# Optimization experiments

Measured on AMD Instinct MI355X. Metric: run time of the kernel, lower is better.

The kernel has to match this reference:

```python
import jax, jax.numpy as jnp
import numpy as np

DIM = 1024
N_HEAD = 16
N_KV_HEAD = 4
HEAD_DIM = DIM // N_HEAD  # 64
INTER = 2688
B, N = 2, 2048
EPS = 1e-6


def setup_inputs() -> dict:
    key = jax.random.key(0)
    ks = jax.random.split(key, 10)
    std = 0.02
    x = jax.random.normal(ks[0], (B, N, DIM), dtype=jnp.float32)
    # rotary embedding: theta = pos * 10000^(-2i/d), cos/sin of shape [N, HEAD_DIM//2]
    inv_freq = 1.0 / (10000.0 ** (np.arange(0, HEAD_DIM, 2, dtype=np.float32) / HEAD_DIM))
    t = np.arange(N, dtype=np.float32)
    ang = np.outer(t, inv_freq)  # [N, HEAD_DIM//2]
    rope_cos = jnp.asarray(np.cos(ang))
    rope_sin = jnp.asarray(np.sin(ang))
    mask = jnp.tril(jnp.ones((N, N), dtype=bool))  # True = attend
    return {
        "x": x,
        "w_attn_norm": jnp.ones((DIM,), jnp.float32),
        "w_ffn_norm": jnp.ones((DIM,), jnp.float32),
        "Wq": jax.random.normal(ks[1], (DIM, N_HEAD * HEAD_DIM), jnp.float32) * std,
        "Wkv": jax.random.normal(ks[2], (DIM, 2 * N_KV_HEAD * HEAD_DIM), jnp.float32) * std,
        "Wo": jax.random.normal(ks[3], (N_HEAD * HEAD_DIM, DIM), jnp.float32) * std,
        "W1": jax.random.normal(ks[4], (DIM, INTER), jnp.float32) * std,
        "W2": jax.random.normal(ks[5], (INTER, DIM), jnp.float32) * std,
        "W3": jax.random.normal(ks[6], (DIM, INTER), jnp.float32) * std,
        "rope_cos": rope_cos,
        "rope_sin": rope_sin,
        "mask": mask,
    }


def _rms_norm(x, w):
    # nn.functional.rms_norm: x / sqrt(mean(x^2) + eps) * w
    return x * jax.lax.rsqrt(jnp.mean(x * x, axis=-1, keepdims=True) + EPS) * w


def _apply_rope(x, cos, sin):
    # x: [b, n, h, d]; consecutive pairs (x[2k], x[2k+1]) form complex numbers
    xr = x[..., 0::2]
    xi = x[..., 1::2]
    c = cos[None, :, None, :]
    s = sin[None, :, None, :]
    yr = xr * c - xi * s
    yi = xr * s + xi * c
    return jnp.stack([yr, yi], axis=-1).reshape(x.shape)


def _block(x, w_attn_norm, w_ffn_norm, Wq, Wkv, Wo, W1, W2, W3, rope_cos, rope_sin, mask):
    b, n, _ = x.shape
    # --- attention (GQA, use_cache=False prefill) ---
    h = _rms_norm(x, w_attn_norm)
    q = (h @ Wq).reshape(b, n, N_HEAD, HEAD_DIM)
    kv = h @ Wkv
    k, v = jnp.split(kv, 2, axis=-1)
    k = k.reshape(b, n, N_KV_HEAD, HEAD_DIM)
    v = v.reshape(b, n, N_KV_HEAD, HEAD_DIM)
    q = _apply_rope(q, rope_cos, rope_sin)
    k = _apply_rope(k, rope_cos, rope_sin)
    # einops repeat 'b n h d -> b n (r h) d' == tile along head axis
    r = N_HEAD // N_KV_HEAD
    k = jnp.tile(k, (1, 1, r, 1))
    v = jnp.tile(v, (1, 1, r, 1))
    scale = HEAD_DIM ** -0.5
    scores = jnp.einsum('bnhd,bmhd->bhnm', q, k) * scale
    scores = jnp.where(mask[None, None, :, :], scores, jnp.finfo(scores.dtype).min)
    attn = jax.nn.softmax(scores, axis=-1)
    o = jnp.einsum('bhnm,bmhd->bnhd', attn, v).reshape(b, n, N_HEAD * HEAD_DIM)
    x = x + o @ Wo
    # --- SwiGLU MLP ---
    h2 = _rms_norm(x, w_ffn_norm)
    ff = (jax.nn.silu(h2 @ W1) * (h2 @ W3)) @ W2
    return x + ff


def reference(x, w_attn_norm, w_ffn_norm, Wq, Wkv, Wo, W1, W2, W3, rope_cos, rope_sin, mask):
    return _block(x, w_attn_norm, w_ffn_norm, Wq, Wkv, Wo, W1, W2, W3, rope_cos, rope_sin, mask)
```

## Files before the change

### kernel.cpp

```cpp
#include <hip/hip_runtime.h>

#define DIM 1024
#define NH 16
#define NKV 4
#define HD 64
#define INTER 2688
#define BB 2
#define NN 2048
#define MM (BB*NN)

typedef __attribute__((ext_vector_type(4))) float f32x4;
typedef __attribute__((ext_vector_type(16))) float f32x16;
typedef __attribute__((ext_vector_type(8))) short short8;

#define CROW(r,h) ((((r)&3)) + 8*((r)>>2) + 4*(h))

__device__ __forceinline__ unsigned short f2bf(float f) {
  union { float f; unsigned u; } v; v.f = f;
  unsigned r = v.u + 0x7fffu + ((v.u >> 16) & 1u);
  return (unsigned short)(r >> 16);
}

__device__ __forceinline__ void glds16(const unsigned short* g, unsigned short* l) {
  __builtin_amdgcn_global_load_lds(
      (const __attribute__((address_space(1))) void*)g,
      (__attribute__((address_space(3))) void*)l, 16, 0, 0);
}

__device__ __forceinline__ void xcd_map(int& bx, int& by) {
  int gx = gridDim.x;
  int nwg = gx * gridDim.y;
  int bid = (int)blockIdx.y * gx + (int)blockIdx.x;
  int cpx = nwg >> 3;
  int lg = (bid & 7) * cpx + (bid >> 3);
  bx = lg % gx;
  by = lg / gx;
}

__global__ void transpose_all(const float* __restrict__ Wq, const float* __restrict__ Wkv,
                              const float* __restrict__ Wo, const float* __restrict__ W1,
                              const float* __restrict__ W3, const float* __restrict__ W2,
                              unsigned short* __restrict__ WqkvT, unsigned short* __restrict__ WoT,
                              unsigned short* __restrict__ W1T, unsigned short* __restrict__ W3T,
                              unsigned short* __restrict__ W2T) {
  int tb = blockIdx.x;
  const float* src; unsigned short* dst; int K, Nc, t0;
  if (tb < 1024)        { src = Wq;  dst = WqkvT;                         K = 1024; Nc = 1024; t0 = tb; }
  else if (tb < 1536)   { src = Wkv; dst = WqkvT + (size_t)1024 * 1024;   K = 1024; Nc = 512;  t0 = tb - 1024; }
  else if (tb < 2560)   { src = Wo;  dst = WoT;                           K = 1024; Nc = 1024; t0 = tb - 1536; }
  else if (tb < 5248)   { src = W1;  dst = W1T;                           K = 1024; Nc = 2688; t0 = tb - 2560; }
  else if (tb < 7936)   { src = W3;  dst = W3T;                           K = 1024; Nc = 2688; t0 = tb - 5248; }
  else                  { src = W2;  dst = W2T;                           K = 2688; Nc = 1024; t0 = tb - 7936; }
  int ntx = Nc >> 5;
  int n0 = (t0 % ntx) * 32, k0 = (t0 / ntx) * 32;
  __shared__ float tile[32][33];
  int tx = threadIdx.x & 31, ty = threadIdx.x >> 5;
#pragma unroll
  for (int i = 0; i < 32; i += 8)
    tile[ty + i][tx] = src[(size_t)(k0 + ty + i) * Nc + n0 + tx];
  __syncthreads();
#pragma unroll
  for (int i = 0; i < 32; i += 8)
    dst[(size_t)(n0 + ty + i) * K + k0 + tx] = f2bf(tile[tx][ty + i]);
}

__global__ void rmsnorm_k(const float* __restrict__ x, const float* __restrict__ w,
                          unsigned short* __restrict__ h) {
  int row = blockIdx.x;
  int t = threadIdx.x;
  const float4* xr = (const float4*)(x + (size_t)row * DIM);
  float4 v = xr[t];
  float ss = v.x * v.x + v.y * v.y + v.z * v.z + v.w * v.w;
#pragma unroll
  for (int o = 1; o < 64; o <<= 1) ss += __shfl_xor(ss, o);
  __shared__ float ps[4];
  if ((t & 63) == 0) ps[t >> 6] = ss;
  __syncthreads();
  float r = rsqrtf((ps[0] + ps[1] + ps[2] + ps[3]) * (1.0f / DIM) + 1e-6f);
  const float4* wr = (const float4*)w;
  float4 wv = wr[t];
  ushort4 o4;
  o4.x = f2bf(v.x * r * wv.x);
  o4.y = f2bf(v.y * r * wv.y);
  o4.z = f2bf(v.z * r * wv.z);
  o4.w = f2bf(v.w * r * wv.w);
  *(ushort4*)(h + (size_t)row * DIM + t * 4) = o4;
}

template <bool RES>
__global__ __launch_bounds__(256, 4) void gemm64(
    const unsigned short* __restrict__ A, const unsigned short* __restrict__ Bt,
    const float* __restrict__ res, float* __restrict__ C, int Nc, int K) {
  __shared__ __align__(16) unsigned short Asm[2][64 * 32];
  __shared__ __align__(16) unsigned short Bsm[2][128 * 32];
  int tid = threadIdx.x;
  int w = tid >> 6, l = tid & 63;
  int bx, by;
  xcd_map(bx, by);
  int bm = by * 64, bn = bx * 128;
  int wc = w * 32;
  int c0 = l & 15, g = l >> 4;

  int sra = w * 16 + (l >> 2);
  int srb = w * 32 + (l >> 2);
  int sca = ((l & 3) ^ ((sra >> 1) & 3)) * 8;
  int scb = ((l & 3) ^ ((srb >> 1) & 3)) * 8;
  const unsigned short* gA  = A + (size_t)(bm + sra) * K + sca;
  const unsigned short* gB0 = Bt + (size_t)(bn + srb) * K + scb;
  const unsigned short* gB1 = Bt + (size_t)(bn + srb + 16) * K + scb;
  int lsa = (w * 16) * 32, lsb0 = (w * 32) * 32, lsb1 = (w * 32 + 16) * 32;

  int aoff[4], boff[2];
#pragma unroll
  for (int m = 0; m < 4; m++) {
    int ra = m * 16 + c0;
    aoff[m] = ra * 32 + (g ^ ((ra >> 1) & 3)) * 8;
  }
#pragma unroll
  for (int n = 0; n < 2; n++) {
    int rb = wc + n * 16 + c0;
    boff[n] = rb * 32 + (g ^ ((rb >> 1) & 3)) * 8;
  }

  f32x4 acc[4][2] = {};
  int T = K / 32;
  glds16(gA, &Asm[0][lsa]);
  glds16(gB0, &Bsm[0][lsb0]);
  glds16(gB1, &Bsm[0][lsb1]);
  __syncthreads();
  int buf = 0;
  for (int s = 0; s < T; ++s) {
    int nb = buf ^ 1;
    if (s + 1 < T) {
      int ko = (s + 1) * 32;
      glds16(gA + ko, &Asm[nb][lsa]);
      glds16(gB0 + ko, &Bsm[nb][lsb0]);
      glds16(gB1 + ko, &Bsm[nb][lsb1]);
    }
    const unsigned short* As = Asm[buf];
    const unsigned short* Bs = Bsm[buf];
    short8 af[4], bf[2];
#pragma unroll
    for (int m = 0; m < 4; m++) af[m] = *(const short8*)&As[aoff[m]];
#pragma unroll
    for (int n = 0; n < 2; n++) bf[n] = *(const short8*)&Bs[boff[n]];
    __builtin_amdgcn_s_setprio(1);
#pragma unroll
    for (int m = 0; m < 4; m++)
#pragma unroll
      for (int n = 0; n < 2; n++)
        acc[m][n] = __builtin_amdgcn_mfma_f32_16x16x32_bf16(af[m], bf[n], acc[m][n], 0, 0, 0);
    __builtin_amdgcn_s_setprio(0);
    __syncthreads();
    buf = nb;
  }
  int gq = l >> 4;
#pragma unroll
  for (int m = 0; m < 4; m++) {
#pragma unroll
    for (int i = 0; i < 4; i++) {
      int row = bm + m * 16 + gq * 4 + i;
#pragma unroll
      for (int n = 0; n < 2; n++) {
        int col = bn + wc + n * 16 + c0;
        float v = acc[m][n][i];
        if (RES) v += res[(size_t)row * Nc + col];
        C[(size_t)row * Nc + col] = v;
      }
    }
  }
}

__global__ __launch_bounds__(256, 4) void gemm_qkv(
    const unsigned short* __restrict__ A, const unsigned short* __restrict__ Bt,
    const float* __restrict__ cosb, const float* __restrict__ sinb,
    unsigned short* __restrict__ qb, unsigned short* __restrict__ kb,
    unsigned short* __restrict__ vtb) {
  const int K = 1024;
  const float QS = 0.125f * 1.44269504f;
  __shared__ __align__(16) unsigned short Asm[2][64 * 32];
  __shared__ __align__(16) unsigned short Bsm[2][128 * 32];
  int tid = threadIdx.x;
  int w = tid >> 6, l = tid & 63;
  int bx, by;
  xcd_map(bx, by);
  int bm = by * 64, bn = bx * 128;
  int wc = w * 32;
  int c0 = l & 15, g = l >> 4;

  int sra = w * 16 + (l >> 2);
  int srb = w * 32 + (l >> 2);
  int sca = ((l & 3) ^ ((sra >> 1) & 3)) * 8;
  int scb = ((l & 3) ^ ((srb >> 1) & 3)) * 8;
  const unsigned short* gA  = A + (size_t)(bm + sra) * K + sca;
  const unsigned short* gB0 = Bt + (size_t)(bn + srb) * K + scb;
  const unsigned short* gB1 = Bt + (size_t)(bn + srb + 16) * K + scb;
  int lsa = (w * 16) * 32, lsb0 = (w * 32) * 32, lsb1 = (w * 32 + 16) * 32;

  int aoff[4], boff[2];
#pragma unroll
  for (int m = 0; m < 4; m++) {
    int ra = m * 16 + c0;
    aoff[m] = ra * 32 + (g ^ ((ra >> 1) & 3)) * 8;
  }
#pragma unroll
  for (int n = 0; n < 2; n++) {
    int rb = wc + n * 16 + c0;
    boff[n] = rb * 32 + (g ^ ((rb >> 1) & 3)) * 8;
  }

  f32x4 acc[4][2] = {};
  int T = K / 32;
  glds16(gA, &Asm[0][lsa]);
  glds16(gB0, &Bsm[0][lsb0]);
  glds16(gB1, &Bsm[0][lsb1]);
  __syncthreads();
  int buf = 0;
  for (int s = 0; s < T; ++s) {
    int nb = buf ^ 1;
    if (s + 1 < T) {
      int ko = (s + 1) * 32;
      glds16(gA + ko, &Asm[nb][lsa]);
      glds16(gB0 + ko, &Bsm[nb][lsb0]);
      glds16(gB1 + ko, &Bsm[nb][lsb1]);
    }
    const unsigned short* As = Asm[buf];
    const unsigned short* Bs = Bsm[buf];
    short8 af[4], bf[2];
#pragma unroll
    for (int m = 0; m < 4; m++) af[m] = *(const short8*)&As[aoff[m]];
#pragma unroll
    for (int n = 0; n < 2; n++) bf[n] = *(const short8*)&Bs[boff[n]];
    __builtin_amdgcn_s_setprio(1);
#pragma unroll
    for (int m = 0; m < 4; m++)
#pragma unroll
      for (int n = 0; n < 2; n++)
        acc[m][n] = __builtin_amdgcn_mfma_f32_16x16x32_bf16(af[m], bf[n], acc[m][n], 0, 0, 0);
    __builtin_amdgcn_s_setprio(0);
    __syncthreads();
    buf = nb;
  }
  int gq = l >> 4;
  int lodd = c0 & 1;
#pragma unroll
  for (int m = 0; m < 4; m++) {
#pragma unroll
    for (int i = 0; i < 4; i++) {
      int row = bm + m * 16 + gq * 4 + i;
      int b = row >> 11, tok = row & (NN - 1);
#pragma unroll
      for (int n = 0; n < 2; n++) {
        int col = bn + wc + n * 16 + c0;
        float val = acc[m][n][i];
        float partner = __shfl_xor(val, 1);
        if (bn < 1024) {
          int head = col >> 6, d = col & 63, j = d >> 1;
          float c = cosb[tok * 32 + j], s = sinb[tok * 32 + j];
          float r = lodd ? (partner * s + val * c) : (val * c - partner * s);
          qb[(((size_t)(b * NH + head)) * NN + tok) * 64 + d] = f2bf(r * QS);
        } else if (bn < 1280) {
          int cc = col - 1024;
          int kvh = cc >> 6, d = cc & 63, j = d >> 1;
          float c = cosb[tok * 32 + j], s = sinb[tok * 32 + j];
          float r = lodd ? (partner * s + val * c) : (val * c - partner * s);
          kb[(((size_t)(b * NKV + kvh)) * NN + tok) * 64 + d] = f2bf(r);
        } else {
          int cc = col - 1280;
          int kvh = cc >> 6, d = cc & 63;
          vtb[(((size_t)(b * NKV + kvh)) * 64 + d) * NN + tok] = f2bf(val);
        }
      }
    }
  }
}

__global__ __launch_bounds__(256, 3) void gemm_ffn13(
    const unsigned short* __restrict__ A, const unsigned short* __restrict__ B1t,
    const unsigned short* __restrict__ B3t, unsigned short* __restrict__ G,
    int Nc, int K) {
  __shared__ __align__(16) unsigned short Asm[2 * 128 * 32];
  __shared__ __align__(16) unsigned short B1sm[2 * 64 * 32];
  __shared__ __align__(16) unsigned short B3sm[2 * 64 * 32];
  int tid = threadIdx.x;
  int w = tid >> 6, l = tid & 63;
  int bm = blockIdx.y * 128, bn = blockIdx.x * 64;
  int wr = (w >> 1) * 64, wc = (w & 1) * 32;
  int c0 = l & 15, g = l >> 4;

  int sr = w * 32 + (l >> 2);
  int sb = w * 16 + (l >> 2);
  int sc  = ((l & 3) ^ ((sr >> 1) & 3)) * 8;
  int scb = ((l & 3) ^ ((sb >> 1) & 3)) * 8;
  const unsigned short* gA0 = A + (size_t)(bm + sr) * K + sc;
  const unsigned short* gA1 = A + (size_t)(bm + sr + 16) * K + sc;
  const unsigned short* gB1 = B1t + (size_t)(bn + sb) * K + scb;
  const unsigned short* gB3 = B3t + (size_t)(bn + sb) * K + scb;
  int ls0 = (w * 32) * 32, ls1 = (w * 32 + 16) * 32, lsb = (w * 16) * 32;

  int aoff[4], boff[2];
#pragma unroll
  for (int m = 0; m < 4; m++) {
    int ra = wr + m * 16 + c0;
    aoff[m] = ra * 32 + (g ^ ((ra >> 1) & 3)) * 8;
  }
#pragma unroll
  for (int n = 0; n < 2; n++) {
    int rb = wc + n * 16 + c0;
    boff[n] = rb * 32 + (g ^ ((rb >> 1) & 3)) * 8;
  }

  f32x4 a1[4][2] = {};
  f32x4 a3[4][2] = {};
  int nsteps = K / 32;
  glds16(gA0, &Asm[ls0]);
  glds16(gA1, &Asm[ls1]);
  glds16(gB1, &B1sm[lsb]);
  glds16(gB3, &B3sm[lsb]);
  __syncthreads();
  int buf = 0;
  for (int s = 0; s < nsteps; ++s) {
    int nb = buf ^ 1;
    if (s + 1 < nsteps) {
      int ko = (s + 1) * 32;
      glds16(gA0 + ko, &Asm[nb * 4096 + ls0]);
      glds16(gA1 + ko, &Asm[nb * 4096 + ls1]);
      glds16(gB1 + ko, &B1sm[nb * 2048 + lsb]);
      glds16(gB3 + ko, &B3sm[nb * 2048 + lsb]);
    }
    const unsigned short* As = &Asm[buf * 4096];
    const unsigned short* B1s = &B1sm[buf * 2048];
    const unsigned short* B3s = &B3sm[buf * 2048];
    short8 af[4], b1f[2], b3f[2];
#pragma unroll
    for (int m = 0; m < 4; m++) af[m] = *(const short8*)&As[aoff[m]];
#pragma unroll
    for (int n = 0; n < 2; n++) {
      b1f[n] = *(const short8*)&B1s[boff[n]];
      b3f[n] = *(const short8*)&B3s[boff[n]];
    }
    __builtin_amdgcn_s_setprio(1);
#pragma unroll
    for (int m = 0; m < 4; m++)
#pragma unroll
      for (int n = 0; n < 2; n++) {
        a1[m][n] = __builtin_amdgcn_mfma_f32_16x16x32_bf16(af[m], b1f[n], a1[m][n], 0, 0, 0);
        a3[m][n] = __builtin_amdgcn_mfma_f32_16x16x32_bf16(af[m], b3f[n], a3[m][n], 0, 0, 0);
      }
    __builtin_amdgcn_s_setprio(0);
    __syncthreads();
    buf = nb;
  }
  int gq = l >> 4;
#pragma unroll
  for (int m = 0; m < 4; m++) {
#pragma unroll
    for (int i = 0; i < 4; i++) {
      int row = bm + wr + m * 16 + gq * 4 + i;
#pragma unroll
      for (int n = 0; n < 2; n++) {
        int col = bn + wc + n * 16 + c0;
        float x1 = a1[m][n][i], x3 = a3[m][n][i];
        float sg = x1 / (1.0f + __expf(-x1));
        G[(size_t)row * Nc + col] = f2bf(sg * x3);
      }
    }
  }
}

__global__ __launch_bounds__(256, 3) void attn_k(
    const unsigned short* __restrict__ qg_, const unsigned short* __restrict__ kg_,
    const unsigned short* __restrict__ vg_, unsigned short* __restrict__ ob) {
  __shared__ __align__(16) unsigned short Ksm[2][64 * 64];
  __shared__ __align__(16) unsigned short Vsm[2][64 * 64];
  int qb = (blockIdx.z == 0) ? (int)blockIdx.x : ((int)gridDim.x - 1 - (int)blockIdx.x);
  int h = blockIdx.y, b = blockIdx.z;
  int kvh = h & 3;
  int tid = threadIdx.x, w = tid >> 6, l = tid & 63;
  int q5 = l & 31, hi = l >> 5;
  int qwbase = qb * 128 + w * 32;
  int qgl = qwbase + q5;

  const unsigned short* Kg = kg_ + ((size_t)(b * NKV + kvh)) * NN * 64;
  const unsigned short* Vg = vg_ + ((size_t)(b * NKV + kvh)) * 64 * NN;

  short8 qf[4];
  {
    const unsigned short* qrow = qg_ + (((size_t)(b * NH + h)) * NN + qgl) * 64 + hi * 8;
#pragma unroll
    for (int d = 0; d < 4; d++) qf[d] = *(const short8*)(qrow + d * 16);
  }

  int srow = l >> 3;
  int schunk = (l & 7) ^ (srow & 7);
  const unsigned short* gK = Kg + (size_t)(w * 16 + srow) * 64 + schunk * 8;
  const unsigned short* gV = Vg + (size_t)(w * 16 + srow) * NN + schunk * 8;

  int nkt = qb * 2 + 2;
  int nkt_w = ((qwbase + 31) >> 6) + 1;

  f32x16 O0 = {}, O1 = {};
  float m_r = -1e30f, l_r = 0.0f;

  glds16(gK, &Ksm[0][w * 1024]);
  glds16(gK + 8 * 64, &Ksm[0][w * 1024 + 512]);
  glds16(gV, &Vsm[0][w * 1024]);
  glds16(gV + 8 * NN, &Vsm[0][w * 1024 + 512]);
  __syncthreads();

  int buf = 0;
  for (int kt = 0; kt < nkt; ++kt) {
    int n0 = kt * 64;
    if (kt + 1 < nkt) {
      int nb = buf ^ 1;
      glds16(gK + (size_t)(n0 + 64) * 64, &Ksm[nb][w * 1024]);
      glds16(gK + (size_t)(n0 + 64) * 64 + 8 * 64, &Ksm[nb][w * 1024 + 512]);
      glds16(gV + n0 + 64, &Vsm[nb][w * 1024]);
      glds16(gV + 8 * NN + n0 + 64, &Vsm[nb][w * 1024 + 512]);
    }
    if (kt < nkt_w) {
      const unsigned short* Ks = Ksm[buf];
      const unsigned short* Vs = Vsm[buf];
      f32x16 S[2];
      __builtin_amdgcn_s_setprio(1);
#pragma unroll
      for (int s = 0; s < 2; s++) {
        f32x16 acc = {};
        int row = s * 32 + q5;
#pragma unroll
        for (int d = 0; d < 4; d++) {
          int ch = (2 * d + hi) ^ (row & 7);
          short8 kf = *(const short8*)&Ks[row * 64 + ch * 8];
          acc = __builtin_amdgcn_mfma_f32_32x32x16_bf16(kf, qf[d], acc, 0, 0, 0);
        }
        S[s] = acc;
      }
      __builtin_amdgcn_s_setprio(0);
      if (kt == nkt_w - 1) {
#pragma unroll
        for (int s = 0; s < 2; s++)
#pragma unroll
          for (int r = 0; r < 16; r++) {
            int kg = n0 + s * 32 + CROW(r, hi);
            S[s][r] = (kg > qgl) ? -1e30f : S[s][r];
          }
      }
      float t16[16];
#pragma unroll
      for (int r = 0; r < 16; r++) t16[r] = fmaxf(S[0][r], S[1][r]);
#pragma unroll
      for (int k = 8; k >= 1; k >>= 1)
#pragma unroll
        for (int r = 0; r < k; r++) t16[r] = fmaxf(t16[r], t16[r + k]);
      float pm = fmaxf(t16[0], __shfl_xor(t16[0], 32));
      if (!__all(pm <= m_r + 8.0f)) {
        float mn = fmaxf(m_r, pm);
        float alpha = exp2f(m_r - mn);
        m_r = mn;
        l_r *= alpha;
        float ab[16];
#pragma unroll
        for (int r = 0; r < 16; r++) ab[r] = __shfl(alpha, CROW(r, 0) + 4 * hi);
#pragma unroll
        for (int r = 0; r < 16; r++) { O0[r] *= ab[r]; O1[r] *= ab[r]; }
      }
#pragma unroll
      for (int s = 0; s < 2; s++)
#pragma unroll
        for (int r = 0; r < 16; r++) S[s][r] = exp2f(S[s][r] - m_r);
      float u[16];
#pragma unroll
      for (int r = 0; r < 16; r++) u[r] = S[0][r] + S[1][r];
#pragma unroll
      for (int k = 8; k >= 1; k >>= 1)
#pragma unroll
        for (int r = 0; r < k; r++) u[r] += u[r + k];
      l_r += (u[0] + __shfl_xor(u[0], 32));
      short8 paf[4];
#pragma unroll
      for (int ks = 0; ks < 4; ks++) {
        const int s = ks >> 1, e = ks & 1;
        unsigned a0, a1, b0, b1;
        asm("v_cvt_pk_bf16_f32 %0, %1, %2" : "=v"(a0) : "v"(S[s][8*e+0]), "v"(S[s][8*e+1]));
        asm("v_cvt_pk_bf16_f32 %0, %1, %2" : "=v"(a1) : "v"(S[s][8*e+2]), "v"(S[s][8*e+3]));
        asm("v_cvt_pk_bf16_f32 %0, %1, %2" : "=v"(b0) : "v"(S[s][8*e+4]), "v"(S[s][8*e+5]));
        asm("v_cvt_pk_bf16_f32 %0, %1, %2" : "=v"(b1) : "v"(S[s][8*e+6]), "v"(S[s][8*e+7]));
        asm("v_permlane32_swap_b32 %0, %1" : "+v"(a0), "+v"(b0));
        asm("v_permlane32_swap_b32 %0, %1" : "+v"(a1), "+v"(b1));
        union { unsigned u4[4]; short8 s8; } pk;
        pk.u4[0] = a0; pk.u4[1] = a1; pk.u4[2] = b0; pk.u4[3] = b1;
        paf[ks] = pk.s8;
      }
      __builtin_amdgcn_s_setprio(1);
#pragma unroll
      for (int ks = 0; ks < 4; ks++) {
        int row0 = q5, row1 = 32 + q5;
        short8 vf0 = *(const short8*)&Vs[row0 * 64 + (((2 * ks + hi) ^ (row0 & 7)) * 8)];
        short8 vf1 = *(const short8*)&Vs[row1 * 64 + (((2 * ks + hi) ^ (row1 & 7)) * 8)];
        O0 = __builtin_amdgcn_mfma_f32_32x32x16_bf16(paf[ks], vf0, O0, 0, 0, 0);
        O1 = __builtin_amdgcn_mfma_f32_32x32x16_bf16(paf[ks], vf1, O1, 0, 0, 0);
      }
      __builtin_amdgcn_s_setprio(0);
    }
    __syncthreads();
    buf ^= 1;
  }
  float linv = 1.0f / l_r;
  float lb[16];
#pragma unroll
  for (int r = 0; r < 16; r++) lb[r] = __shfl(linv, CROW(r, 0) + 4 * hi);
#pragma unroll
  for (int r = 0; r < 16; r++) {
    int orow = qwbase + CROW(r, hi);
    size_t base = ((size_t)b * NN + orow) * 1024 + h * 64 + q5;
    ob[base] = f2bf(O0[r] * lb[r]);
    ob[base + 32] = f2bf(O1[r] * lb[r]);
  }
}

extern "C" void kernel_launch(void* const* d_in, const int* in_sizes, int n_in,
                              void* d_out, int out_size, void* d_ws, size_t ws_size,
                              hipStream_t stream) {
  (void)in_sizes; (void)n_in; (void)out_size; (void)ws_size;
  const float* x    = (const float*)d_in[0];
  const float* w_an = (const float*)d_in[1];
  const float* w_fn = (const float*)d_in[2];
  const float* Wq   = (const float*)d_in[3];
  const float* Wkv  = (const float*)d_in[4];
  const float* Wo   = (const float*)d_in[5];
  const float* W1   = (const float*)d_in[6];
  const float* W2   = (const float*)d_in[7];
  const float* W3   = (const float*)d_in[8];
  const float* cosb = (const float*)d_in[9];
  const float* sinb = (const float*)d_in[10];
  float* out = (float*)d_out;

  char* ws = (char*)d_ws;
  size_t off = 0;
  auto take = [&](size_t bytes) {
    size_t r = off;
    off += (bytes + 255) & ~(size_t)255;
    return r;
  };
  unsigned short* WqkvT = (unsigned short*)(ws + take((size_t)1536 * 1024 * 2));
  unsigned short* WoT   = (unsigned short*)(ws + take((size_t)1024 * 1024 * 2));
  unsigned short* W1T   = (unsigned short*)(ws + take((size_t)2688 * 1024 * 2));
  unsigned short* W3T   = (unsigned short*)(ws + take((size_t)2688 * 1024 * 2));
  unsigned short* W2T   = (unsigned short*)(ws + take((size_t)2688 * 1024 * 2));
  unsigned short* hA    = (unsigned short*)(ws + take((size_t)MM * DIM * 2));
  unsigned short* gbuf  = (unsigned short*)(ws + take((size_t)MM * INTER * 2));
  unsigned short* qbuf = (unsigned short*)(ws + take((size_t)MM * DIM * 2));
  unsigned short* kbuf = (unsigned short*)(ws + take((size_t)BB * NKV * NN * HD * 2));
  unsigned short* vtb  = (unsigned short*)(ws + take((size_t)BB * NKV * NN * HD * 2));
  unsigned short* obuf = (unsigned short*)(ws + take((size_t)MM * DIM * 2));
  float* x2 = (float*)(ws + take((size_t)MM * DIM * 4));

  transpose_all<<<10624, 256, 0, stream>>>(Wq, Wkv, Wo, W1, W3, W2,
                                           WqkvT, WoT, W1T, W3T, W2T);
  rmsnorm_k<<<MM, 256, 0, stream>>>(x, w_an, hA);
  gemm_qkv<<<dim3(1536 / 128, MM / 64), 256, 0, stream>>>(hA, WqkvT, cosb, sinb,
                                                          qbuf, kbuf, vtb);
  attn_k<<<dim3(NN / 128, NH, BB), 256, 0, stream>>>(qbuf, kbuf, vtb, obuf);
  gemm64<true><<<dim3(1024 / 128, MM / 64), 256, 0, stream>>>(obuf, WoT, x, x2, 1024, 1024);
  rmsnorm_k<<<MM, 256, 0, stream>>>(x2, w_fn, hA);
  gemm_ffn13<<<dim3(INTER / 64, MM / 128), 256, 0, stream>>>(hA, W1T, W3T, gbuf, INTER, 1024);
  gemm64<true><<<dim3(1024 / 128, MM / 64), 256, 0, stream>>>(gbuf, W2T, x2, out, 1024, 2688);
}
```

Measured before the change: 238.4 us.

## Deepen GEMM K-tile to 64, store residual stream in bf16, retune launch bounds

The gemm64 and gemm_qkv kernels now stage 64-wide K slices in shared memory with a new XOR swizzle and two MFMA substeps per tile. This halves the number of barrier-separated iterations at the cost of doubled LDS and lower occupancy bounds. The intermediate residual x2 is now stored in bf16 instead of fp32, cutting its write and read traffic in the Wo GEMM, the second rmsnorm and the W2 GEMM. This adds rounding error to the residual path. The launch bounds for gemm_ffn13 are also raised to 4 blocks.

```diff
diff --git a/kernel.cpp b/kernel.cpp
--- a/kernel.cpp
+++ b/kernel.cpp
@@ -20,6 +20,13 @@
   unsigned r = v.u + 0x7fffu + ((v.u >> 16) & 1u);
   return (unsigned short)(r >> 16);
 }
+__device__ __forceinline__ float bf2f(unsigned short u) {
+  union { unsigned u; float f; } v; v.u = ((unsigned)u) << 16; return v.f;
+}
+__device__ __forceinline__ float ld_res(const float* p) { return *p; }
+__device__ __forceinline__ float ld_res(const unsigned short* p) { return bf2f(*p); }
+__device__ __forceinline__ void st_out(float* p, float v) { *p = v; }
+__device__ __forceinline__ void st_out(unsigned short* p, float v) { *p = f2bf(v); }
 
 __device__ __forceinline__ void glds16(const unsigned short* g, unsigned short* l) {
   __builtin_amdgcn_global_load_lds(
@@ -64,12 +71,18 @@
     dst[(size_t)(n0 + ty + i) * K + k0 + tx] = f2bf(tile[tx][ty + i]);
 }
 
-__global__ void rmsnorm_k(const float* __restrict__ x, const float* __restrict__ w,
+template <typename InT>
+__global__ void rmsnorm_k(const InT* __restrict__ x, const float* __restrict__ w,
                           unsigned short* __restrict__ h) {
   int row = blockIdx.x;
   int t = threadIdx.x;
-  const float4* xr = (const float4*)(x + (size_t)row * DIM);
-  float4 v = xr[t];
+  float4 v;
+  if constexpr (sizeof(InT) == 4) {
+    v = ((const float4*)(x + (size_t)row * DIM))[t];
+  } else {
+    ushort4 u = ((const ushort4*)(x + (size_t)row * DIM))[t];
+    v.x = bf2f(u.x); v.y = bf2f(u.y); v.z = bf2f(u.z); v.w = bf2f(u.w);
+  }
   float ss = v.x * v.x + v.y * v.y + v.z * v.z + v.w * v.w;
 #pragma unroll
   for (int o = 1; o < 64; o <<= 1) ss += __shfl_xor(ss, o);
@@ -77,8 +90,7 @@
   if ((t & 63) == 0) ps[t >> 6] = ss;
   __syncthreads();
   float r = rsqrtf((ps[0] + ps[1] + ps[2] + ps[3]) * (1.0f / DIM) + 1e-6f);
-  const float4* wr = (const float4*)w;
-  float4 wv = wr[t];
+  float4 wv = ((const float4*)w)[t];
   ushort4 o4;
   o4.x = f2bf(v.x * r * wv.x);
   o4.y = f2bf(v.y * r * wv.y);
@@ -87,12 +99,12 @@
   *(ushort4*)(h + (size_t)row * DIM + t * 4) = o4;
 }
 
-template <bool RES>
-__global__ __launch_bounds__(256, 4) void gemm64(
+template <typename ResT, typename OutT>
+__global__ __launch_bounds__(256, 3) void gemm64(
     const unsigned short* __restrict__ A, const unsigned short* __restrict__ Bt,
-    const float* __restrict__ res, float* __restrict__ C, int Nc, int K) {
-  __shared__ __align__(16) unsigned short Asm[2][64 * 32];
-  __shared__ __align__(16) unsigned short Bsm[2][128 * 32];
+    const ResT* __restrict__ res, OutT* __restrict__ C, int Nc, int K) {
+  __shared__ __align__(16) unsigned short Asm[2][64 * 64];
+  __shared__ __align__(16) unsigned short Bsm[2][128 * 64];
   int tid = threadIdx.x;
   int w = tid >> 6, l = tid & 63;
   int bx, by;
@@ -101,56 +113,57 @@
   int wc = w * 32;
   int c0 = l & 15, g = l >> 4;
 
-  int sra = w * 16 + (l >> 2);
-  int srb = w * 32 + (l >> 2);
-  int sca = ((l & 3) ^ ((sra >> 1) & 3)) * 8;
-  int scb = ((l & 3) ^ ((srb >> 1) & 3)) * 8;
-  const unsigned short* gA  = A + (size_t)(bm + sra) * K + sca;
-  const unsigned short* gB0 = Bt + (size_t)(bn + srb) * K + scb;
-  const unsigned short* gB1 = Bt + (size_t)(bn + srb + 16) * K + scb;
-  int lsa = (w * 16) * 32, lsb0 = (w * 32) * 32, lsb1 = (w * 32 + 16) * 32;
-
-  int aoff[4], boff[2];
-#pragma unroll
-  for (int m = 0; m < 4; m++) {
-    int ra = m * 16 + c0;
-    aoff[m] = ra * 32 + (g ^ ((ra >> 1) & 3)) * 8;
-  }
-#pragma unroll
-  for (int n = 0; n < 2; n++) {
-    int rb = wc + n * 16 + c0;
-    boff[n] = rb * 32 + (g ^ ((rb >> 1) & 3)) * 8;
-  }
+  int sra = w * 16 + (l >> 3);
+  int srb = w * 32 + (l >> 3);
+  int schA = ((l & 7) ^ (l >> 3)) * 8;
+  const unsigned short* gA = A + (size_t)(bm + sra) * K + schA;
+  const unsigned short* gB = Bt + (size_t)(bn + srb) * K + schA;
+  int lsa = (w * 16) * 64, lsb = (w * 32) * 64;
 
   f32x4 acc[4][2] = {};
-  int T = K / 32;
+  int T = K / 64;
   glds16(gA, &Asm[0][lsa]);
-  glds16(gB0, &Bsm[0][lsb0]);
-  glds16(gB1, &Bsm[0][lsb1]);
+  glds16(gA + 8 * K, &Asm[0][lsa + 8 * 64]);
+  glds16(gB, &Bsm[0][lsb]);
+  glds16(gB + 8 * K, &Bsm[0][lsb + 8 * 64]);
+  glds16(gB + 16 * K, &Bsm[0][lsb + 16 * 64]);
+  glds16(gB + 24 * K, &Bsm[0][lsb + 24 * 64]);
   __syncthreads();
   int buf = 0;
   for (int s = 0; s < T; ++s) {
     int nb = buf ^ 1;
     if (s + 1 < T) {
-      int ko = (s + 1) * 32;
+      int ko = (s + 1) * 64;
       glds16(gA + ko, &Asm[nb][lsa]);
-      glds16(gB0 + ko, &Bsm[nb][lsb0]);
-      glds16(gB1 + ko, &Bsm[nb][lsb1]);
+      glds16(gA + 8 * K + ko, &Asm[nb][lsa + 8 * 64]);
+      glds16(gB + ko, &Bsm[nb][lsb]);
+      glds16(gB + 8 * K + ko, &Bsm[nb][lsb + 8 * 64]);
+      glds16(gB + 16 * K + ko, &Bsm[nb][lsb + 16 * 64]);
+      glds16(gB + 24 * K + ko, &Bsm[nb][lsb + 24 * 64]);
     }
     const unsigned short* As = Asm[buf];
     const unsigned short* Bs = Bsm[buf];
-    short8 af[4], bf[2];
-#pragma unroll
-    for (int m = 0; m < 4; m++) af[m] = *(const short8*)&As[aoff[m]];
-#pragma unroll
-    for (int n = 0; n < 2; n++) bf[n] = *(const short8*)&Bs[boff[n]];
-    __builtin_amdgcn_s_setprio(1);
-#pragma unroll
-    for (int m = 0; m < 4; m++)
-#pragma unroll
-      for (int n = 0; n < 2; n++)
-        acc[m][n] = __builtin_amdgcn_mfma_f32_16x16x32_bf16(af[m], bf[n], acc[m][n], 0, 0, 0);
-    __builtin_amdgcn_s_setprio(0);
+#pragma unroll
+    for (int ks = 0; ks < 2; ++ks) {
+      short8 af[4], bf[2];
+#pragma unroll
+      for (int m = 0; m < 4; m++) {
+        int ra = m * 16 + c0;
+        af[m] = *(const short8*)&As[ra * 64 + (((ks * 4 + g) ^ (ra & 7)) * 8)];
+      }
+#pragma unroll
+      for (int n = 0; n < 2; n++) {
+        int rb = wc + n * 16 + c0;
+        bf[n] = *(const short8*)&Bs[rb * 64 + (((ks * 4 + g) ^ (rb & 7)) * 8)];
+      }
+      __builtin_amdgcn_s_setprio(1);
+#pragma unroll
+      for (int m = 0; m < 4; m++)
+#pragma unroll
+        for (int n = 0; n < 2; n++)
+          acc[m][n] = __builtin_amdgcn_mfma_f32_16x16x32_bf16(af[m], bf[n], acc[m][n], 0, 0, 0);
+      __builtin_amdgcn_s_setprio(0);
+    }
     __syncthreads();
     buf = nb;
   }
@@ -163,23 +176,22 @@
 #pragma unroll
       for (int n = 0; n < 2; n++) {
         int col = bn + wc + n * 16 + c0;
-        float v = acc[m][n][i];
-        if (RES) v += res[(size_t)row * Nc + col];
-        C[(size_t)row * Nc + col] = v;
-      }
-    }
-  }
-}
-
-__global__ __launch_bounds__(256, 4) void gemm_qkv(
+        float v = acc[m][n][i] + ld_res(&res[(size_t)row * Nc + col]);
+        st_out(&C[(size_t)row * Nc + col], v);
+      }
+    }
+  }
+}
+
+__global__ __launch_bounds__(256, 3) void gemm_qkv(
     const unsigned short* __restrict__ A, const unsigned short* __restrict__ Bt,
     const float* __restrict__ cosb, const float* __restrict__ sinb,
     unsigned short* __restrict__ qb, unsigned short* __restrict__ kb,
     unsigned short* __restrict__ vtb) {
   const int K = 1024;
   const float QS = 0.125f * 1.44269504f;
-  __shared__ __align__(16) unsigned short Asm[2][64 * 32];
-  __shared__ __align__(16) unsigned short Bsm[2][128 * 32];
+  __shared__ __align__(16) unsigned short Asm[2][64 * 64];
+  __shared__ __align__(16) unsigned short Bsm[2][128 * 64];
   int tid = threadIdx.x;
   int w = tid >> 6, l = tid & 63;
   int bx, by;
@@ -188,56 +200,57 @@
   int wc = w * 32;
   int c0 = l & 15, g = l >> 4;
 
-  int sra = w * 16 + (l >> 2);
-  int srb = w * 32 + (l >> 2);
-  int sca = ((l & 3) ^ ((sra >> 1) & 3)) * 8;
-  int scb = ((l & 3) ^ ((srb >> 1) & 3)) * 8;
-  const unsigned short* gA  = A + (size_t)(bm + sra) * K + sca;
-  const unsigned short* gB0 = Bt + (size_t)(bn + srb) * K + scb;
-  const unsigned short* gB1 = Bt + (size_t)(bn + srb + 16) * K + scb;
-  int lsa = (w * 16) * 32, lsb0 = (w * 32) * 32, lsb1 = (w * 32 + 16) * 32;
-
-  int aoff[4], boff[2];
-#pragma unroll
-  for (int m = 0; m < 4; m++) {
-    int ra = m * 16 + c0;
-    aoff[m] = ra * 32 + (g ^ ((ra >> 1) & 3)) * 8;
-  }
-#pragma unroll
-  for (int n = 0; n < 2; n++) {
-    int rb = wc + n * 16 + c0;
-    boff[n] = rb * 32 + (g ^ ((rb >> 1) & 3)) * 8;
-  }
+  int sra = w * 16 + (l >> 3);
+  int srb = w * 32 + (l >> 3);
+  int schA = ((l & 7) ^ (l >> 3)) * 8;
+  const unsigned short* gA = A + (size_t)(bm + sra) * K + schA;
+  const unsigned short* gB = Bt + (size_t)(bn + srb) * K + schA;
+  int lsa = (w * 16) * 64, lsb = (w * 32) * 64;
 
   f32x4 acc[4][2] = {};
-  int T = K / 32;
+  int T = K / 64;
   glds16(gA, &Asm[0][lsa]);
-  glds16(gB0, &Bsm[0][lsb0]);
-  glds16(gB1, &Bsm[0][lsb1]);
+  glds16(gA + 8 * K, &Asm[0][lsa + 8 * 64]);
+  glds16(gB, &Bsm[0][lsb]);
+  glds16(gB + 8 * K, &Bsm[0][lsb + 8 * 64]);
+  glds16(gB + 16 * K, &Bsm[0][lsb + 16 * 64]);
+  glds16(gB + 24 * K, &Bsm[0][lsb + 24 * 64]);
   __syncthreads();
   int buf = 0;
   for (int s = 0; s < T; ++s) {
     int nb = buf ^ 1;
     if (s + 1 < T) {
-      int ko = (s + 1) * 32;
+      int ko = (s + 1) * 64;
       glds16(gA + ko, &Asm[nb][lsa]);
-      glds16(gB0 + ko, &Bsm[nb][lsb0]);
-      glds16(gB1 + ko, &Bsm[nb][lsb1]);
+      glds16(gA + 8 * K + ko, &Asm[nb][lsa + 8 * 64]);
+      glds16(gB + ko, &Bsm[nb][lsb]);
+      glds16(gB + 8 * K + ko, &Bsm[nb][lsb + 8 * 64]);
+      glds16(gB + 16 * K + ko, &Bsm[nb][lsb + 16 * 64]);
+      glds16(gB + 24 * K + ko, &Bsm[nb][lsb + 24 * 64]);
     }
     const unsigned short* As = Asm[buf];
     const unsigned short* Bs = Bsm[buf];
-    short8 af[4], bf[2];
-#pragma unroll
-    for (int m = 0; m < 4; m++) af[m] = *(const short8*)&As[aoff[m]];
-#pragma unroll
-    for (int n = 0; n < 2; n++) bf[n] = *(const short8*)&Bs[boff[n]];
-    __builtin_amdgcn_s_setprio(1);
-#pragma unroll
-    for (int m = 0; m < 4; m++)
-#pragma unroll
-      for (int n = 0; n < 2; n++)
-        acc[m][n] = __builtin_amdgcn_mfma_f32_16x16x32_bf16(af[m], bf[n], acc[m][n], 0, 0, 0);
-    __builtin_amdgcn_s_setprio(0);
+#pragma unroll
+    for (int ks = 0; ks < 2; ++ks) {
+      short8 af[4], bf[2];
+#pragma unroll
+      for (int m = 0; m < 4; m++) {
+        int ra = m * 16 + c0;
+        af[m] = *(const short8*)&As[ra * 64 + (((ks * 4 + g) ^ (ra & 7)) * 8)];
+      }
+#pragma unroll
+      for (int n = 0; n < 2; n++) {
+        int rb = wc + n * 16 + c0;
+        bf[n] = *(const short8*)&Bs[rb * 64 + (((ks * 4 + g) ^ (rb & 7)) * 8)];
+      }
+      __builtin_amdgcn_s_setprio(1);
+#pragma unroll
+      for (int m = 0; m < 4; m++)
+#pragma unroll
+        for (int n = 0; n < 2; n++)
+          acc[m][n] = __builtin_amdgcn_mfma_f32_16x16x32_bf16(af[m], bf[n], acc[m][n], 0, 0, 0);
+      __builtin_amdgcn_s_setprio(0);
+    }
     __syncthreads();
     buf = nb;
   }
@@ -275,7 +288,7 @@
   }
 }
 
-__global__ __launch_bounds__(256, 3) void gemm_ffn13(
+__global__ __launch_bounds__(256, 4) void gemm_ffn13(
     const unsigned short* __restrict__ A, const unsigned short* __restrict__ B1t,
     const unsigned short* __restrict__ B3t, unsigned short* __restrict__ G,
     int Nc, int K) {
@@ -553,16 +566,18 @@
   unsigned short* kbuf = (unsigned short*)(ws + take((size_t)BB * NKV * NN * HD * 2));
   unsigned short* vtb  = (unsigned short*)(ws + take((size_t)BB * NKV * NN * HD * 2));
   unsigned short* obuf = (unsigned short*)(ws + take((size_t)MM * DIM * 2));
-  float* x2 = (float*)(ws + take((size_t)MM * DIM * 4));
+  unsigned short* x2b  = (unsigned short*)(ws + take((size_t)MM * DIM * 2));
 
   transpose_all<<<10624, 256, 0, stream>>>(Wq, Wkv, Wo, W1, W3, W2,
                                            WqkvT, WoT, W1T, W3T, W2T);
-  rmsnorm_k<<<MM, 256, 0, stream>>>(x, w_an, hA);
+  rmsnorm_k<float><<<MM, 256, 0, stream>>>(x, w_an, hA);
   gemm_qkv<<<dim3(1536 / 128, MM / 64), 256, 0, stream>>>(hA, WqkvT, cosb, sinb,
                                                           qbuf, kbuf, vtb);
   attn_k<<<dim3(NN / 128, NH, BB), 256, 0, stream>>>(qbuf, kbuf, vtb, obuf);
-  gemm64<true><<<dim3(1024 / 128, MM / 64), 256, 0, stream>>>(obuf, WoT, x, x2, 1024, 1024);
-  rmsnorm_k<<<MM, 256, 0, stream>>>(x2, w_fn, hA);
+  gemm64<float, unsigned short><<<dim3(1024 / 128, MM / 64), 256, 0, stream>>>(
+      obuf, WoT, x, x2b, 1024, 1024);
+  rmsnorm_k<unsigned short><<<MM, 256, 0, stream>>>(x2b, w_fn, hA);
   gemm_ffn13<<<dim3(INTER / 64, MM / 128), 256, 0, stream>>>(hA, W1T, W3T, gbuf, INTER, 1024);
-  gemm64<true><<<dim3(1024 / 128, MM / 64), 256, 0, stream>>>(gbuf, W2T, x2, out, 1024, 2688);
-}
+  gemm64<unsigned short, float><<<dim3(1024 / 128, MM / 64), 256, 0, stream>>>(
+      gbuf, W2T, x2b, out, 1024, 2688);
+}
```

New measurement: 221.3 us. 1.08x faster.
